# Performance work log

Measured on AMD Instinct MI355X. Metric: run time of the kernel, lower is better.

The kernel has to match this reference:

```python
import jax, jax.numpy as jnp
import numpy as np
from math import sqrt

HEADS = 16
DIM_HEAD = 64
BETA = 1.0 / sqrt(DIM_HEAD)


def setup_inputs() -> dict:
    key = jax.random.key(0)
    k1, k2, k3 = jax.random.split(key, 3)
    b, n, dim = 2, 2048, 1024
    inner = HEADS * DIM_HEAD  # 1024
    x = jax.random.normal(k1, (b, n, dim), dtype=jnp.float32)
    W_qk = jax.random.normal(k2, (dim, 2 * inner), dtype=jnp.float32) * 0.02
    W_out = jax.random.normal(k3, (inner, dim), dtype=jnp.float32) * 0.02
    return {"x": x, "W_qk": W_qk, "W_out": W_out}


def reference(x, W_qk, W_out):
    # x: [b, n, dim]; to_qk: Linear(dim, 2*inner, bias=False)
    b, n, _ = x.shape
    qk = x @ W_qk                                   # [b, n, 2*inner]
    q, k = jnp.split(qk, 2, axis=-1)                # each [b, n, inner]
    # b n (h d) -> b h n d
    q = q.reshape(b, n, HEADS, DIM_HEAD).transpose(0, 2, 1, 3)
    k = k.reshape(b, n, HEADS, DIM_HEAD).transpose(0, 2, 1, 3)
    # beta-scaled scores
    scores = jnp.einsum('bhid,bhjd->bhij', q * BETA, k)  # [b, h, n, n]
    mask_value = -jnp.finfo(scores.dtype).max
    causal_mask = jnp.triu(jnp.ones((n, n), dtype=bool), k=1)
    scores = jnp.where(causal_mask, mask_value, scores)
    attn = jax.nn.softmax(scores, axis=-1)
    # K is reused as V
    out = jnp.einsum('bhij,bhjd->bhid', attn, k)    # [b, h, n, d]
    out = out.transpose(0, 2, 1, 3).reshape(b, n, HEADS * DIM_HEAD)
    # to_out Linear (dropout is identity in eval)
    return out @ W_out
```

## Files before the change

kernel.cpp:

```cpp
#include <hip/hip_runtime.h>
#include <hip/hip_bf16.h>
#include <math.h>

typedef short bf16x8 __attribute__((ext_vector_type(8)));
typedef float f32x4 __attribute__((ext_vector_type(4)));

__device__ __forceinline__ float bf2f(unsigned short u) {
    return __uint_as_float(((unsigned int)u) << 16);
}
__device__ __forceinline__ unsigned short f2bf(float f) {
    unsigned int u = __float_as_uint(f);
    u = (u + 0x7FFFu + ((u >> 16) & 1u)) >> 16;
    return (unsigned short)u;
}
__device__ __forceinline__ unsigned int pk2bf(float a, float b) {
    __hip_bfloat162 u = __float22bfloat162_rn(make_float2(a, b));
    return *(unsigned int*)&u;
}

#define ASYNC16(gp, lp)                                                        \
    __builtin_amdgcn_global_load_lds(                                          \
        (const __attribute__((address_space(1))) unsigned int*)(gp),           \
        (__attribute__((address_space(3))) unsigned int*)(lp), 16, 0, 0)

__global__ __launch_bounds__(256) void cast_x_kernel(const float* __restrict__ in,
                                                     unsigned short* __restrict__ out, int n) {
    int i = (blockIdx.x * 256 + threadIdx.x) * 8;
    if (i >= n) return;
    float4 a = *(const float4*)(in + i);
    float4 b = *(const float4*)(in + i + 4);
    bf16x8 v;
    v[0] = (short)f2bf(a.x); v[1] = (short)f2bf(a.y); v[2] = (short)f2bf(a.z); v[3] = (short)f2bf(a.w);
    v[4] = (short)f2bf(b.x); v[5] = (short)f2bf(b.y); v[6] = (short)f2bf(b.z); v[7] = (short)f2bf(b.w);
    *(bf16x8*)(out + i) = v;
}

__global__ __launch_bounds__(256) void transpose_cast_kernel(const float* __restrict__ in,
                                                             unsigned short* __restrict__ out,
                                                             int K, int N) {
    __shared__ float tile[32][33];
    int k0 = blockIdx.x * 32, n0 = blockIdx.y * 32;
    int tx = threadIdx.x & 31, ty = threadIdx.x >> 5;
    #pragma unroll
    for (int i = ty; i < 32; i += 8)
        tile[i][tx] = in[(size_t)(k0 + i) * N + (n0 + tx)];
    __syncthreads();
    #pragma unroll
    for (int i = ty; i < 32; i += 8)
        out[(size_t)(n0 + i) * K + (k0 + tx)] = f2bf(tile[tx][i]);
}

__global__ __launch_bounds__(256) void ktrans_kernel(const unsigned short* __restrict__ qkb,
                                                     unsigned short* __restrict__ kT) {
    __shared__ unsigned short tl[64][68];
    const int b = blockIdx.z;
    const int tok0 = blockIdx.x * 64;
    const int f0 = blockIdx.y * 64;
    const int r = threadIdx.x >> 4;
    const int c = (threadIdx.x & 15) * 4;
    #pragma unroll
    for (int i = 0; i < 4; ++i) {
        const int rr = r + 16 * i;
        ushort4 v = *(const ushort4*)(qkb + ((size_t)(b * 2048 + tok0 + rr)) * 2048 + 1024 + f0 + c);
        *(ushort4*)&tl[rr][c] = v;
    }
    __syncthreads();
    #pragma unroll
    for (int i = 0; i < 4; ++i) {
        const int fr = r + 16 * i;
        ushort4 v;
        v.x = tl[c + 0][fr]; v.y = tl[c + 1][fr]; v.z = tl[c + 2][fr]; v.w = tl[c + 3][fr];
        *(ushort4*)(kT + ((size_t)(b * 1024 + f0 + fr)) * 2048 + tok0 + c) = v;
    }
}

template <bool STORE_BF16>
__global__ __launch_bounds__(256) void gemm128_kernel(const unsigned short* __restrict__ A,
                                                      const unsigned short* __restrict__ Bt,
                                                      void* __restrict__ C,
                                                      int K, int lda, int ldb, int ldc) {
    __shared__ unsigned short As[128 * 32];
    __shared__ unsigned short Bs[128 * 32];
    const int tid = threadIdx.x;
    const int wave = tid >> 6;
    const int lane = tid & 63;
    const int quad = lane >> 4;
    const int col  = lane & 15;
    const int wm = (wave >> 1) * 64;
    const int wn = (wave & 1) * 64;
    const int m0 = blockIdx.x * 128, n0 = blockIdx.y * 128;

    f32x4 acc[4][4];
    #pragma unroll
    for (int i = 0; i < 4; ++i)
        #pragma unroll
        for (int j = 0; j < 4; ++j) { acc[i][j][0] = 0.f; acc[i][j][1] = 0.f; acc[i][j][2] = 0.f; acc[i][j][3] = 0.f; }

    const int srow = tid >> 2;
    const int skc  = (tid & 3) * 8;

    for (int k0 = 0; k0 < K; k0 += 32) {
        __syncthreads();
        const unsigned short* ga = A  + (size_t)(m0 + srow) * lda + k0 + skc;
        const unsigned short* gb = Bt + (size_t)(n0 + srow) * ldb + k0 + skc;
        ASYNC16(ga,            &As[wave * 512]);
        ASYNC16(ga + 64 * lda, &As[2048 + wave * 512]);
        ASYNC16(gb,            &Bs[wave * 512]);
        ASYNC16(gb + 64 * ldb, &Bs[2048 + wave * 512]);
        __syncthreads();

        bf16x8 af[4], bf[4];
        #pragma unroll
        for (int mf = 0; mf < 4; ++mf)
            af[mf] = *(const bf16x8*)&As[(wm + mf * 16 + col) * 32 + quad * 8];
        #pragma unroll
        for (int nf = 0; nf < 4; ++nf)
            bf[nf] = *(const bf16x8*)&Bs[(wn + nf * 16 + col) * 32 + quad * 8];
        #pragma unroll
        for (int mf = 0; mf < 4; ++mf)
            #pragma unroll
            for (int nf = 0; nf < 4; ++nf)
                acc[mf][nf] = __builtin_amdgcn_mfma_f32_16x16x32_bf16(af[mf], bf[nf], acc[mf][nf], 0, 0, 0);
    }

    #pragma unroll
    for (int mf = 0; mf < 4; ++mf) {
        const int row0 = m0 + wm + mf * 16 + quad * 4;
        #pragma unroll
        for (int nf = 0; nf < 4; ++nf) {
            const int cc = n0 + wn + nf * 16 + col;
            #pragma unroll
            for (int r = 0; r < 4; ++r) {
                if (STORE_BF16)
                    ((unsigned short*)C)[(size_t)(row0 + r) * ldc + cc] = f2bf(acc[mf][nf][r]);
                else
                    ((float*)C)[(size_t)(row0 + r) * ldc + cc] = acc[mf][nf][r];
            }
        }
    }
}

__global__ __launch_bounds__(256, 4) void attn_v9_kernel(const unsigned short* __restrict__ qkb,
                                                         const unsigned short* __restrict__ kT,
                                                         unsigned short* __restrict__ aout) {
    __shared__ unsigned short Kbuf[2][2][64 * 64];
    __shared__ unsigned short Ps[4][16 * 64];

    const int bh = blockIdx.x;
    const int b = bh >> 4, h = bh & 15;
    const int qtile = 31 - (int)blockIdx.y;
    const int tid = threadIdx.x;
    const int wave = tid >> 6, lane = tid & 63, quad = lane >> 4, col = lane & 15;
    const int sw = col & 7;

    bf16x8 qa0, qa1;
    {
        const unsigned short* qp =
            qkb + ((size_t)(b * 2048 + qtile * 64 + wave * 16 + col)) * 2048 + h * 64;
        bf16x8 r0 = *(const bf16x8*)(qp + quad * 8);
        bf16x8 r1 = *(const bf16x8*)(qp + 32 + quad * 8);
        const float sc = 0.125f * 1.44269504088896f;
        #pragma unroll
        for (int i = 0; i < 8; ++i) {
            qa0[i] = (short)f2bf(bf2f((unsigned short)r0[i]) * sc);
            qa1[i] = (short)f2bf(bf2f((unsigned short)r1[i]) * sc);
        }
    }

    f32x4 accO[4];
    #pragma unroll
    for (int t = 0; t < 4; ++t) { accO[t][0] = 0.f; accO[t][1] = 0.f; accO[t][2] = 0.f; accO[t][3] = 0.f; }
    float lsum = 0.f;

    const int r8 = lane >> 3;
    const int c8 = (lane & 7) ^ r8;
    const unsigned short* knp =
        qkb + ((size_t)(b * 2048 + wave * 16 + r8)) * 2048 + 1024 + h * 64 + c8 * 8;
    const unsigned short* ktp = kT + ((size_t)(bh * 64 + wave * 16 + r8)) * 2048 + c8 * 8;

    auto issue = [&](int jt, int p) {
        const unsigned short* kn = knp + (size_t)jt * 64 * 2048;
        const unsigned short* kt = ktp + jt * 64;
        unsigned short* knl = &Kbuf[p][0][(wave * 16) * 64];
        unsigned short* ktl = &Kbuf[p][1][(wave * 16) * 64];
        ASYNC16(kn,            knl);
        ASYNC16(kn + 8 * 2048, knl + 8 * 64);
        ASYNC16(kt,            ktl);
        ASYNC16(kt + 8 * 2048, ktl + 8 * 64);
    };

    issue(0, 0);

    for (int jt = 0; jt <= qtile; ++jt) {
        const int cur = jt & 1;
        __builtin_amdgcn_s_barrier();
        if (jt < qtile) issue(jt + 1, cur ^ 1);
        if (jt < qtile) __builtin_amdgcn_s_waitcnt(0xF74);
        else            __builtin_amdgcn_s_waitcnt(0xF70);
        __builtin_amdgcn_s_barrier();
        __asm__ volatile("" ::: "memory");

        const unsigned short* Knc = &Kbuf[cur][0][0];
        const unsigned short* Ktc = &Kbuf[cur][1][0];

        const bool diag = (jt == qtile);
        const int tmax = diag ? wave : 3;

        float ls = 0.f;
        unsigned int pw[4][2];
        #pragma unroll
        for (int t = 0; t < 4; ++t) {
            if (t <= tmax) {
                const int row = (t * 16 + col) * 64;
                bf16x8 ka0 = *(const bf16x8*)&Knc[row + (quad ^ sw) * 8];
                bf16x8 ka1 = *(const bf16x8*)&Knc[row + ((4 + quad) ^ sw) * 8];
                f32x4 c = {-16.f, -16.f, -16.f, -16.f};
                c = __builtin_amdgcn_mfma_f32_16x16x32_bf16(ka0, qa0, c, 0, 0, 0);
                c = __builtin_amdgcn_mfma_f32_16x16x32_bf16(ka1, qa1, c, 0, 0, 0);
                if (diag && t == wave) {
                    #pragma unroll
                    for (int r = 0; r < 4; ++r)
                        if (quad * 4 + r > col) c[r] = -1e30f;
                }
                const float p0 = exp2f(c[0]);
                const float p1 = exp2f(c[1]);
                const float p2 = exp2f(c[2]);
                const float p3 = exp2f(c[3]);
                ls += (p0 + p1) + (p2 + p3);
                pw[t][0] = pk2bf(p0, p1);
                pw[t][1] = pk2bf(p2, p3);
            } else {
                pw[t][0] = 0u; pw[t][1] = 0u;
            }
        }
        lsum += ls;

        unsigned short* psb = &Ps[wave][col * 64];
        #pragma unroll
        for (int t = 0; t < 4; ++t)
            *(uint2*)(psb + ((2 * t + (quad >> 1)) ^ sw) * 8 + (quad & 1) * 4) =
                make_uint2(pw[t][0], pw[t][1]);

        bf16x8 pa0 = *(const bf16x8*)(psb + (quad ^ sw) * 8);
        bf16x8 pa1 = *(const bf16x8*)(psb + ((4 + quad) ^ sw) * 8);
        const bool hi = !(diag && wave < 2);

        #pragma unroll
        for (int t = 0; t < 4; ++t) {
            const int row = (t * 16 + col) * 64;
            bf16x8 vb0 = *(const bf16x8*)&Ktc[row + (quad ^ sw) * 8];
            accO[t] = __builtin_amdgcn_mfma_f32_16x16x32_bf16(pa0, vb0, accO[t], 0, 0, 0);
            if (hi) {
                bf16x8 vb1 = *(const bf16x8*)&Ktc[row + ((4 + quad) ^ sw) * 8];
                accO[t] = __builtin_amdgcn_mfma_f32_16x16x32_bf16(pa1, vb1, accO[t], 0, 0, 0);
            }
        }
    }

    lsum += __shfl_xor(lsum, 16);
    lsum += __shfl_xor(lsum, 32);
    #pragma unroll
    for (int r = 0; r < 4; ++r) {
        const float lr = __shfl(lsum, (lane & 48) | (quad * 4 + r));
        const float inv = 1.f / lr;
        const size_t row = (size_t)b * 2048 + qtile * 64 + wave * 16 + quad * 4 + r;
        unsigned short* op = aout + row * 1024 + h * 64;
        op[col]      = f2bf(accO[0][r] * inv);
        op[16 + col] = f2bf(accO[1][r] * inv);
        op[32 + col] = f2bf(accO[2][r] * inv);
        op[48 + col] = f2bf(accO[3][r] * inv);
    }
}

extern "C" void kernel_launch(void* const* d_in, const int* in_sizes, int n_in,
                              void* d_out, int out_size, void* d_ws, size_t ws_size,
                              hipStream_t stream) {
    (void)in_sizes; (void)n_in; (void)out_size; (void)ws_size;
    const float* x    = (const float*)d_in[0];
    const float* Wqk  = (const float*)d_in[1];
    const float* Wout = (const float*)d_in[2];
    float* out = (float*)d_out;

    unsigned short* xb     = (unsigned short*)d_ws;
    unsigned short* Wqk_t  = xb     + (size_t)4096 * 1024;
    unsigned short* Wout_t = Wqk_t  + (size_t)2048 * 1024;
    unsigned short* qkb    = Wout_t + (size_t)1024 * 1024;
    unsigned short* aoutb  = qkb    + (size_t)4096 * 2048;
    unsigned short* kT     = xb;

    cast_x_kernel<<<dim3(4096 * 1024 / (256 * 8)), dim3(256), 0, stream>>>(x, xb, 4096 * 1024);
    transpose_cast_kernel<<<dim3(32, 64), dim3(256), 0, stream>>>(Wqk, Wqk_t, 1024, 2048);
    transpose_cast_kernel<<<dim3(32, 32), dim3(256), 0, stream>>>(Wout, Wout_t, 1024, 1024);

    gemm128_kernel<true><<<dim3(32, 16), dim3(256), 0, stream>>>(
        xb, Wqk_t, (void*)qkb, 1024, 1024, 1024, 2048);

    ktrans_kernel<<<dim3(32, 16, 2), dim3(256), 0, stream>>>(qkb, kT);

    attn_v9_kernel<<<dim3(32, 32), dim3(256), 0, stream>>>(qkb, kT, aoutb);

    gemm128_kernel<false><<<dim3(32, 8), dim3(256), 0, stream>>>(
        aoutb, Wout_t, (void*)out, 1024, 1024, 1024, 1024);
}
```

Measured before the change: 191.6 us.

## Load V fragments directly from global memory and add MFMA priority hints

The attention kernel stops staging the transposed K (used as V) tile in LDS. Each wave now loads its V MFMA operands straight from global/L2 per tile, which halves the LDS footprint and raises the occupancy hint from 4 to 6 blocks per CU. s_setprio is placed around the MFMA groups, and the waitcnt is adjusted for the smaller number of async loads. The cost is that each wave issues redundant, uncoalesced global loads of V with latency exposed inside the loop, since they are not prefetched a tile ahead.

```diff
diff --git a/kernel.cpp b/kernel.cpp
--- a/kernel.cpp
+++ b/kernel.cpp
@@ -140,10 +140,10 @@
     }
 }
 
-__global__ __launch_bounds__(256, 4) void attn_v9_kernel(const unsigned short* __restrict__ qkb,
-                                                         const unsigned short* __restrict__ kT,
-                                                         unsigned short* __restrict__ aout) {
-    __shared__ unsigned short Kbuf[2][2][64 * 64];
+__global__ __launch_bounds__(256, 6) void attn_v10_kernel(const unsigned short* __restrict__ qkb,
+                                                          const unsigned short* __restrict__ kT,
+                                                          unsigned short* __restrict__ aout) {
+    __shared__ unsigned short Kbuf[2][64 * 64];
     __shared__ unsigned short Ps[4][16 * 64];
 
     const int bh = blockIdx.x;
@@ -176,17 +176,14 @@
     const int c8 = (lane & 7) ^ r8;
     const unsigned short* knp =
         qkb + ((size_t)(b * 2048 + wave * 16 + r8)) * 2048 + 1024 + h * 64 + c8 * 8;
-    const unsigned short* ktp = kT + ((size_t)(bh * 64 + wave * 16 + r8)) * 2048 + c8 * 8;
+
+    const unsigned short* vtile = kT + ((size_t)(bh * 64 + col)) * 2048 + quad * 8;
 
     auto issue = [&](int jt, int p) {
         const unsigned short* kn = knp + (size_t)jt * 64 * 2048;
-        const unsigned short* kt = ktp + jt * 64;
-        unsigned short* knl = &Kbuf[p][0][(wave * 16) * 64];
-        unsigned short* ktl = &Kbuf[p][1][(wave * 16) * 64];
+        unsigned short* knl = &Kbuf[p][(wave * 16) * 64];
         ASYNC16(kn,            knl);
         ASYNC16(kn + 8 * 2048, knl + 8 * 64);
-        ASYNC16(kt,            ktl);
-        ASYNC16(kt + 8 * 2048, ktl + 8 * 64);
     };
 
     issue(0, 0);
@@ -195,13 +192,19 @@
         const int cur = jt & 1;
         __builtin_amdgcn_s_barrier();
         if (jt < qtile) issue(jt + 1, cur ^ 1);
-        if (jt < qtile) __builtin_amdgcn_s_waitcnt(0xF74);
+        __asm__ volatile("" ::: "memory");
+        if (jt < qtile) __builtin_amdgcn_s_waitcnt(0xF72);
         else            __builtin_amdgcn_s_waitcnt(0xF70);
         __builtin_amdgcn_s_barrier();
         __asm__ volatile("" ::: "memory");
 
-        const unsigned short* Knc = &Kbuf[cur][0][0];
-        const unsigned short* Ktc = &Kbuf[cur][1][0];
+        const unsigned short* Knc = &Kbuf[cur][0];
+        const unsigned short* vj = vtile + jt * 64;
+
+        bf16x8 vlo[4];
+        #pragma unroll
+        for (int t = 0; t < 4; ++t)
+            vlo[t] = *(const bf16x8*)(vj + t * 16 * 2048);
 
         const bool diag = (jt == qtile);
         const int tmax = diag ? wave : 3;
@@ -215,8 +218,10 @@
                 bf16x8 ka0 = *(const bf16x8*)&Knc[row + (quad ^ sw) * 8];
                 bf16x8 ka1 = *(const bf16x8*)&Knc[row + ((4 + quad) ^ sw) * 8];
                 f32x4 c = {-16.f, -16.f, -16.f, -16.f};
+                __builtin_amdgcn_s_setprio(1);
                 c = __builtin_amdgcn_mfma_f32_16x16x32_bf16(ka0, qa0, c, 0, 0, 0);
                 c = __builtin_amdgcn_mfma_f32_16x16x32_bf16(ka1, qa1, c, 0, 0, 0);
+                __builtin_amdgcn_s_setprio(0);
                 if (diag && t == wave) {
                     #pragma unroll
                     for (int r = 0; r < 4; ++r)
@@ -245,15 +250,22 @@
         bf16x8 pa1 = *(const bf16x8*)(psb + ((4 + quad) ^ sw) * 8);
         const bool hi = !(diag && wave < 2);
 
-        #pragma unroll
-        for (int t = 0; t < 4; ++t) {
-            const int row = (t * 16 + col) * 64;
-            bf16x8 vb0 = *(const bf16x8*)&Ktc[row + (quad ^ sw) * 8];
-            accO[t] = __builtin_amdgcn_mfma_f32_16x16x32_bf16(pa0, vb0, accO[t], 0, 0, 0);
-            if (hi) {
-                bf16x8 vb1 = *(const bf16x8*)&Ktc[row + ((4 + quad) ^ sw) * 8];
-                accO[t] = __builtin_amdgcn_mfma_f32_16x16x32_bf16(pa1, vb1, accO[t], 0, 0, 0);
-            }
+        __builtin_amdgcn_s_setprio(1);
+        #pragma unroll
+        for (int t = 0; t < 4; ++t)
+            accO[t] = __builtin_amdgcn_mfma_f32_16x16x32_bf16(pa0, vlo[t], accO[t], 0, 0, 0);
+        __builtin_amdgcn_s_setprio(0);
+
+        if (hi) {
+            bf16x8 vhi[4];
+            #pragma unroll
+            for (int t = 0; t < 4; ++t)
+                vhi[t] = *(const bf16x8*)(vj + t * 16 * 2048 + 32);
+            __builtin_amdgcn_s_setprio(1);
+            #pragma unroll
+            for (int t = 0; t < 4; ++t)
+                accO[t] = __builtin_amdgcn_mfma_f32_16x16x32_bf16(pa1, vhi[t], accO[t], 0, 0, 0);
+            __builtin_amdgcn_s_setprio(0);
         }
     }
 
@@ -297,7 +309,7 @@
 
     ktrans_kernel<<<dim3(32, 16, 2), dim3(256), 0, stream>>>(qkb, kT);
 
-    attn_v9_kernel<<<dim3(32, 32), dim3(256), 0, stream>>>(qkb, kT, aoutb);
+    attn_v10_kernel<<<dim3(32, 32), dim3(256), 0, stream>>>(qkb, kT, aoutb);
 
     gemm128_kernel<false><<<dim3(32, 8), dim3(256), 0, stream>>>(
         aoutb, Wout_t, (void*)out, 1024, 1024, 1024, 1024);
```

Result: slower. 245.9 us (+28.3%).

## Software-pipeline PV matmul one tile behind QK and compute row sums via MFMA

Applied to the files above, without the earlier changes.

Restructures the attention loop so the P·V MFMAs for the previous key tile are issued right after the current tile's QK MFMAs, which lets the exp2 and LDS round-trip of the current tile overlap with matrix work. The P and V fragments are kept in registers across iterations. The row-sum normalizer is now accumulated with an extra MFMA against a vector of ones, replacing the scalar adds and cross-lane shuffles. It also raises wave priority around the MFMA block. The cost is more live registers (V fragments, previous P) and the loss of the diagonal half-skip on the PV MFMA. The row sum is now taken from bf16-rounded probabilities, which matches the numerator more closely.

```diff
diff --git a/kernel.cpp b/kernel.cpp
--- a/kernel.cpp
+++ b/kernel.cpp
@@ -140,9 +140,9 @@
     }
 }
 
-__global__ __launch_bounds__(256, 4) void attn_v9_kernel(const unsigned short* __restrict__ qkb,
-                                                         const unsigned short* __restrict__ kT,
-                                                         unsigned short* __restrict__ aout) {
+__global__ __launch_bounds__(256, 4) void attn_v11_kernel(const unsigned short* __restrict__ qkb,
+                                                          const unsigned short* __restrict__ kT,
+                                                          unsigned short* __restrict__ aout) {
     __shared__ unsigned short Kbuf[2][2][64 * 64];
     __shared__ unsigned short Ps[4][16 * 64];
 
@@ -167,10 +167,17 @@
         }
     }
 
+    bf16x8 ones;
+    #pragma unroll
+    for (int i = 0; i < 8; ++i) ones[i] = (short)0x3F80;
+
     f32x4 accO[4];
     #pragma unroll
     for (int t = 0; t < 4; ++t) { accO[t][0] = 0.f; accO[t][1] = 0.f; accO[t][2] = 0.f; accO[t][3] = 0.f; }
-    float lsum = 0.f;
+    f32x4 accL = {0.f, 0.f, 0.f, 0.f};
+
+    bf16x8 pa0p = {}, pa1p = {};
+    bf16x8 vlo[4] = {}, vhi[4] = {};
 
     const int r8 = lane >> 3;
     const int c8 = (lane & 7) ^ r8;
@@ -206,34 +213,51 @@
         const bool diag = (jt == qtile);
         const int tmax = diag ? wave : 3;
 
-        float ls = 0.f;
-        unsigned int pw[4][2];
+        f32x4 c[4];
+        __builtin_amdgcn_s_setprio(1);
         #pragma unroll
         for (int t = 0; t < 4; ++t) {
             if (t <= tmax) {
                 const int row = (t * 16 + col) * 64;
                 bf16x8 ka0 = *(const bf16x8*)&Knc[row + (quad ^ sw) * 8];
                 bf16x8 ka1 = *(const bf16x8*)&Knc[row + ((4 + quad) ^ sw) * 8];
-                f32x4 c = {-16.f, -16.f, -16.f, -16.f};
-                c = __builtin_amdgcn_mfma_f32_16x16x32_bf16(ka0, qa0, c, 0, 0, 0);
-                c = __builtin_amdgcn_mfma_f32_16x16x32_bf16(ka1, qa1, c, 0, 0, 0);
+                f32x4 ci = {-16.f, -16.f, -16.f, -16.f};
+                ci = __builtin_amdgcn_mfma_f32_16x16x32_bf16(ka0, qa0, ci, 0, 0, 0);
+                ci = __builtin_amdgcn_mfma_f32_16x16x32_bf16(ka1, qa1, ci, 0, 0, 0);
+                c[t] = ci;
+            }
+        }
+        if (jt) {
+            #pragma unroll
+            for (int t = 0; t < 4; ++t) {
+                accO[t] = __builtin_amdgcn_mfma_f32_16x16x32_bf16(pa0p, vlo[t], accO[t], 0, 0, 0);
+                accO[t] = __builtin_amdgcn_mfma_f32_16x16x32_bf16(pa1p, vhi[t], accO[t], 0, 0, 0);
+            }
+            accL = __builtin_amdgcn_mfma_f32_16x16x32_bf16(pa0p, ones, accL, 0, 0, 0);
+            accL = __builtin_amdgcn_mfma_f32_16x16x32_bf16(pa1p, ones, accL, 0, 0, 0);
+        }
+        __builtin_amdgcn_s_setprio(0);
+
+        unsigned int pw[4][2];
+        #pragma unroll
+        for (int t = 0; t < 4; ++t) {
+            if (t <= tmax) {
+                f32x4 ci = c[t];
                 if (diag && t == wave) {
                     #pragma unroll
                     for (int r = 0; r < 4; ++r)
-                        if (quad * 4 + r > col) c[r] = -1e30f;
+                        if (quad * 4 + r > col) ci[r] = -1e30f;
                 }
-                const float p0 = exp2f(c[0]);
-                const float p1 = exp2f(c[1]);
-                const float p2 = exp2f(c[2]);
-                const float p3 = exp2f(c[3]);
-                ls += (p0 + p1) + (p2 + p3);
+                const float p0 = exp2f(ci[0]);
+                const float p1 = exp2f(ci[1]);
+                const float p2 = exp2f(ci[2]);
+                const float p3 = exp2f(ci[3]);
                 pw[t][0] = pk2bf(p0, p1);
                 pw[t][1] = pk2bf(p2, p3);
             } else {
                 pw[t][0] = 0u; pw[t][1] = 0u;
             }
         }
-        lsum += ls;
 
         unsigned short* psb = &Ps[wave][col * 64];
         #pragma unroll
@@ -241,28 +265,28 @@
             *(uint2*)(psb + ((2 * t + (quad >> 1)) ^ sw) * 8 + (quad & 1) * 4) =
                 make_uint2(pw[t][0], pw[t][1]);
 
-        bf16x8 pa0 = *(const bf16x8*)(psb + (quad ^ sw) * 8);
-        bf16x8 pa1 = *(const bf16x8*)(psb + ((4 + quad) ^ sw) * 8);
-        const bool hi = !(diag && wave < 2);
+        pa0p = *(const bf16x8*)(psb + (quad ^ sw) * 8);
+        pa1p = *(const bf16x8*)(psb + ((4 + quad) ^ sw) * 8);
 
         #pragma unroll
         for (int t = 0; t < 4; ++t) {
             const int row = (t * 16 + col) * 64;
-            bf16x8 vb0 = *(const bf16x8*)&Ktc[row + (quad ^ sw) * 8];
-            accO[t] = __builtin_amdgcn_mfma_f32_16x16x32_bf16(pa0, vb0, accO[t], 0, 0, 0);
-            if (hi) {
-                bf16x8 vb1 = *(const bf16x8*)&Ktc[row + ((4 + quad) ^ sw) * 8];
-                accO[t] = __builtin_amdgcn_mfma_f32_16x16x32_bf16(pa1, vb1, accO[t], 0, 0, 0);
-            }
-        }
-    }
-
-    lsum += __shfl_xor(lsum, 16);
-    lsum += __shfl_xor(lsum, 32);
+            vlo[t] = *(const bf16x8*)&Ktc[row + (quad ^ sw) * 8];
+            vhi[t] = *(const bf16x8*)&Ktc[row + ((4 + quad) ^ sw) * 8];
+        }
+    }
+
+    #pragma unroll
+    for (int t = 0; t < 4; ++t) {
+        accO[t] = __builtin_amdgcn_mfma_f32_16x16x32_bf16(pa0p, vlo[t], accO[t], 0, 0, 0);
+        accO[t] = __builtin_amdgcn_mfma_f32_16x16x32_bf16(pa1p, vhi[t], accO[t], 0, 0, 0);
+    }
+    accL = __builtin_amdgcn_mfma_f32_16x16x32_bf16(pa0p, ones, accL, 0, 0, 0);
+    accL = __builtin_amdgcn_mfma_f32_16x16x32_bf16(pa1p, ones, accL, 0, 0, 0);
+
     #pragma unroll
     for (int r = 0; r < 4; ++r) {
-        const float lr = __shfl(lsum, (lane & 48) | (quad * 4 + r));
-        const float inv = 1.f / lr;
+        const float inv = 1.f / accL[r];
         const size_t row = (size_t)b * 2048 + qtile * 64 + wave * 16 + quad * 4 + r;
         unsigned short* op = aout + row * 1024 + h * 64;
         op[col]      = f2bf(accO[0][r] * inv);
@@ -297,7 +321,7 @@
 
     ktrans_kernel<<<dim3(32, 16, 2), dim3(256), 0, stream>>>(qkb, kT);
 
-    attn_v9_kernel<<<dim3(32, 32), dim3(256), 0, stream>>>(qkb, kT, aoutb);
+    attn_v11_kernel<<<dim3(32, 32), dim3(256), 0, stream>>>(qkb, kT, aoutb);
 
     gemm128_kernel<false><<<dim3(32, 8), dim3(256), 0, stream>>>(
         aoutb, Wout_t, (void*)out, 1024, 1024, 1024, 1024);
```

New measurement: 183.7 us. -4.2%, faster.
